# Optimization experiments

Hardware: AMD Instinct MI355X
Metric: run time of the kernel (lower is better)

The kernel has to match this reference:

```python
import jax, jax.numpy as jnp
import numpy as np

C = 128      # in_channels == global_graph_width
T = 1024     # time_step_len
B = 32       # batch (scenes)
N = B * T    # total nodes
E = 16 * N   # edges


def setup_inputs() -> dict:
    key = jax.random.key(0)
    ks = jax.random.split(key, 10)
    s = 1.0 / np.sqrt(C)
    return {
        "x": jax.random.normal(ks[0], (N, C), dtype=jnp.float32),
        "edge_index": jax.random.randint(ks[1], (2, E), 0, N, dtype=jnp.int64),
        "valid_lens": jax.random.randint(ks[2], (B,), 1, T, dtype=jnp.int64),
        "time_step_len": T,
        "Wq": jax.random.uniform(ks[3], (C, C), jnp.float32, -s, s),
        "bq": jax.random.uniform(ks[4], (C,), jnp.float32, -s, s),
        "Wk": jax.random.uniform(ks[5], (C, C), jnp.float32, -s, s),
        "bk": jax.random.uniform(ks[6], (C,), jnp.float32, -s, s),
        "Wv": jax.random.uniform(ks[7], (C, C), jnp.float32, -s, s),
        "bv": jax.random.uniform(ks[8], (C,), jnp.float32, -s, s),
    }


def reference(x, edge_index, valid_lens, time_step_len, Wq, bq, Wk, bk, Wv, bv):
    # GlobalGraph.forward in eval mode (no random training mask), 1 layer.
    n_nodes, c = x.shape
    xr = x.reshape(-1, time_step_len, c)                    # [B, T, C]
    q = xr @ Wq.T + bq                                      # [B, T, C]
    k = xr @ Wk.T + bk
    v = xr @ Wv.T + bv
    scores = jnp.einsum("btc,bsc->bts", q, k)               # [B, T, T]
    # masked_softmax: each row (b, t) keeps first valid_lens[b] cols, rest -1e6
    col = jnp.arange(time_step_len)                         # [T]
    mask = col[None, None, :] < valid_lens[:, None, None]   # [B, 1, T]
    scores = jnp.where(mask, scores, -1000000.0)
    attn = jax.nn.softmax(scores, axis=-1)                  # [B, T, T]
    out = jnp.einsum("bts,bsc->btc", attn, v).reshape(-1, c)  # [N, C]
    # MessagePassing propagate, aggr='add', flow source_to_target:
    # out_i = sum_{(j->i) in edges} out_j
    src, dst = edge_index[0], edge_index[1]
    return jax.ops.segment_sum(out[src], dst, num_segments=n_nodes)
```

## Files before the change

### kernel.cpp

```cpp
#include <hip/hip_runtime.h>
#include <hip/hip_bf16.h>
#include <stdint.h>

typedef __attribute__((ext_vector_type(8))) short short8;
typedef __attribute__((ext_vector_type(4))) float f32x4;

static constexpr int NN = 32768;
static constexpr int CC = 128;
static constexpr int TT = 1024;
static constexpr int BB = 32;
static constexpr int EE = 524288;
static constexpr int PAD = 96;
static constexpr int SCH = 512;

__device__ __forceinline__ unsigned short f2b(float f) {
    uint32_t u = __builtin_bit_cast(uint32_t, f);
    u = (u + 0x7fffu + ((u >> 16) & 1u)) >> 16;
    return (unsigned short)u;
}
__device__ __forceinline__ float b2f(unsigned short u) {
    uint32_t v = ((uint32_t)u) << 16;
    return __builtin_bit_cast(float, v);
}

__global__ __launch_bounds__(256) void k_cvtfill(
    const float* __restrict__ Wq, const float* __restrict__ Wk,
    const float* __restrict__ Wv, unsigned short* __restrict__ Wb,
    const int* __restrict__ ei, int* __restrict__ cnt, int* __restrict__ slot)
{
    if (blockIdx.x < 192) {
        int i = blockIdx.x * 256 + threadIdx.x;
        const float* w = (i < CC*CC) ? Wq : ((i < 2*CC*CC) ? Wk : Wv);
        Wb[i] = f2b(w[i & (CC*CC - 1)]);
    } else {
        int e = (blockIdx.x - 192) * 256 + threadIdx.x;
        int src = ei[e];
        int dst = ei[EE + e];
        int pos = atomicAdd(&cnt[dst], 1);
        if (pos < PAD) slot[(size_t)dst * PAD + pos] = src;
    }
}

static constexpr int QP = 132;

__global__ __launch_bounds__(256) void k_qkv(
    const float* __restrict__ x, const unsigned short* __restrict__ Wb,
    const float* __restrict__ bq, const float* __restrict__ bk, const float* __restrict__ bv,
    unsigned short* __restrict__ Qb, unsigned short* __restrict__ Kb,
    unsigned short* __restrict__ VB)
{
    __shared__ unsigned short qsm[4][16 * QP];
    int wv   = threadIdx.x >> 6;
    int wid  = (blockIdx.x << 2) + wv;
    int lane = threadIdx.x & 63;
    int l15  = lane & 15, quad = lane >> 4;
    int m0   = wid << 4;
    unsigned short* myT = qsm[wv];

    short8 a[4];
    const float* xrow = x + (size_t)(m0 + l15) * CC + quad * 8;
#pragma unroll
    for (int kk = 0; kk < 4; kk++) {
        float4 f0 = *(const float4*)(xrow + kk * 32);
        float4 f1 = *(const float4*)(xrow + kk * 32 + 4);
        short8 v;
        v[0] = (short)f2b(f0.x); v[1] = (short)f2b(f0.y);
        v[2] = (short)f2b(f0.z); v[3] = (short)f2b(f0.w);
        v[4] = (short)f2b(f1.x); v[5] = (short)f2b(f1.y);
        v[6] = (short)f2b(f1.z); v[7] = (short)f2b(f1.w);
        a[kk] = v;
    }

    for (int w2 = 0; w2 < 2; w2++) {
        const float* bias = w2 ? bk : bq;
        for (int nt = 0; nt < 8; nt++) {
            int n0 = nt << 4;
            const unsigned short* wbase = Wb + w2 * (CC*CC) + (size_t)(n0 + l15) * CC + quad * 8;
            f32x4 acc = {0.f, 0.f, 0.f, 0.f};
#pragma unroll
            for (int kk = 0; kk < 4; kk++) {
                short8 bfrag = *(const short8*)(wbase + kk * 32);
                acc = __builtin_amdgcn_mfma_f32_16x16x32_bf16(a[kk], bfrag, acc, 0, 0, 0);
            }
            float bval = bias[n0 + l15];
#pragma unroll
            for (int r = 0; r < 4; r++)
                myT[(quad * 4 + r) * QP + n0 + l15] = f2b(acc[r] + bval);
        }
        unsigned short* dstp = w2 ? Kb : Qb;
#pragma unroll
        for (int t = 0; t < 4; t++) {
            int g   = t * 64 + lane;
            int row = g >> 4;
            int gc  = (g & 15) * 8;
            short8 vv = *(const short8*)&myT[row * QP + gc];
            *(short8*)&dstp[(size_t)(m0 + row) * CC + gc] = vv;
        }
    }

    for (int nt = 0; nt < 8; nt++) {
        int n0 = nt << 4;
        const unsigned short* wbase = Wb + 2 * (CC*CC) + (size_t)(n0 + l15) * CC + quad * 8;
        f32x4 acc = {0.f, 0.f, 0.f, 0.f};
#pragma unroll
        for (int kk = 0; kk < 4; kk++) {
            short8 bfrag = *(const short8*)(wbase + kk * 32);
            acc = __builtin_amdgcn_mfma_f32_16x16x32_bf16(a[kk], bfrag, acc, 0, 0, 0);
        }
        float bval = bv[n0 + l15];
        int col = n0 + l15;
        ushort4 pk;
        pk.x = f2b(acc[0] + bval); pk.y = f2b(acc[1] + bval);
        pk.z = f2b(acc[2] + bval); pk.w = f2b(acc[3] + bval);
        int b_  = m0 >> 10;
        int sb  = (m0 & (TT - 1)) >> 5;
        int sin = (m0 & 31) + quad * 4;
        *(ushort4*)&VB[((size_t)(b_ * 32 + sb) * CC + col) * 32 + sin] = pk;
    }
}

static constexpr int PITCH = 40;

__global__ __launch_bounds__(512) void k_attn(
    const unsigned short* __restrict__ Qb, const unsigned short* __restrict__ Kb,
    const unsigned short* __restrict__ VB, const int* __restrict__ valid_lens,
    float* __restrict__ ao_a, float* __restrict__ ao_b,
    float* __restrict__ l0, float* __restrict__ l1,
    unsigned short* __restrict__ ao2)
{
    __shared__ unsigned short Ksm[2][512 * 8];
    __shared__ unsigned short Vsm[2][512 * 8];
    __shared__ unsigned short pl[8][16 * PITCH];

    int w    = threadIdx.x >> 6;
    int lane = threadIdx.x & 63;
    int l15  = lane & 15, quad = lane >> 4;
    int bid   = blockIdx.x;
    int qt8   = bid & 7;
    int chunk = (bid >> 3) & 1;
    int b     = bid >> 4;
    int m0    = b * TT + qt8 * 128 + w * 16;
    int L     = valid_lens[b];
    int sbeg  = chunk * SCH;
    if (sbeg >= L) return;
    int send  = min(L, sbeg + SCH);
    int nsteps = (send - sbeg + 31) >> 5;
    bool excl = (L <= SCH);

    int g    = (w << 6) | lane;
    int ksr  = g >> 4,  ksc = ((g & 15) - ksr) & 15;
    int vch  = g >> 2,  vsg = ((g & 3) - (vch >> 1)) & 3;

    const unsigned short* Kbase = Kb + (size_t)b * TT * CC;
    const unsigned short* Vbase = VB + (size_t)b * 32 * CC * 32;

#define STAGE(bufi, s0g)                                                              \
    do {                                                                              \
        int _s0 = (s0g);                                                              \
        __builtin_amdgcn_global_load_lds(                                             \
            (const __attribute__((address_space(1))) uint32_t*)(Kbase + (size_t)(_s0 + ksr) * CC + ksc * 8), \
            (__attribute__((address_space(3))) uint32_t*)&Ksm[bufi][(size_t)(w << 6) * 8], 16, 0, 0);        \
        const unsigned short* _vt = Vbase + (size_t)(_s0 >> 5) * CC * 32;             \
        __builtin_amdgcn_global_load_lds(                                             \
            (const __attribute__((address_space(1))) uint32_t*)(_vt + vch * 32 + vsg * 8),                   \
            (__attribute__((address_space(3))) uint32_t*)&Vsm[bufi][(size_t)(w << 6) * 8], 16, 0, 0);        \
    } while (0)

    short8 a[4];
    const unsigned short* qrow = Qb + (size_t)(m0 + l15) * CC + quad * 8;
#pragma unroll
    for (int kk = 0; kk < 4; kk++) a[kk] = *(const short8*)(qrow + kk * 32);

    f32x4 o[8];
#pragma unroll
    for (int ct = 0; ct < 8; ct++) o[ct] = (f32x4){0.f, 0.f, 0.f, 0.f};
    float l_[4] = {0.f, 0.f, 0.f, 0.f};

    unsigned short* myP = pl[w];

    STAGE(0, sbeg);
    for (int i = 0; i < nsteps; i++) {
        int s0 = sbeg + (i << 5);
        int bufi = i & 1;
        __syncthreads();
        if (i + 1 < nsteps) STAGE(1 - bufi, s0 + 32);

        const unsigned short* Kc = Ksm[bufi];
        const unsigned short* Vc = Vsm[bufi];

        f32x4 S0 = {0.f,0.f,0.f,0.f}, S1 = {0.f,0.f,0.f,0.f};
#pragma unroll
        for (int kk = 0; kk < 4; kk++) {
            int cidx = kk * 4 + quad;
            int sl0 = l15,      t0 = (cidx + sl0) & 15;
            int sl1 = 16 | l15, t1 = (cidx + sl1) & 15;
            short8 b0 = *(const short8*)&Kc[(size_t)(sl0 * 16 + t0) * 8];
            short8 b1 = *(const short8*)&Kc[(size_t)(sl1 * 16 + t1) * 8];
            S0 = __builtin_amdgcn_mfma_f32_16x16x32_bf16(a[kk], b0, S0, 0, 0, 0);
            S1 = __builtin_amdgcn_mfma_f32_16x16x32_bf16(a[kk], b1, S1, 0, 0, 0);
        }
        bool ok0 = (s0 + l15) < L;
        bool ok1 = (s0 + 16 + l15) < L;
        float p0[4], p1[4];
#pragma unroll
        for (int r = 0; r < 4; r++) {
            p0[r] = ok0 ? __expf(S0[r]) : 0.f;
            p1[r] = ok1 ? __expf(S1[r]) : 0.f;
            l_[r] += p0[r] + p1[r];
        }
#pragma unroll
        for (int r = 0; r < 4; r++) {
            int row = quad * 4 + r;
            myP[row * PITCH + l15]      = f2b(p0[r]);
            myP[row * PITCH + 16 + l15] = f2b(p1[r]);
        }
        short8 pf = *(const short8*)(myP + l15 * PITCH + quad * 8);
#pragma unroll
        for (int ct = 0; ct < 8; ct++) {
            int c  = (ct << 4) | l15;
            int sg = (quad + (c >> 1)) & 3;
            short8 vf = *(const short8*)&Vc[(size_t)(c * 4 + sg) * 8];
            o[ct] = __builtin_amdgcn_mfma_f32_16x16x32_bf16(pf, vf, o[ct], 0, 0, 0);
        }
    }

#pragma unroll
    for (int r = 0; r < 4; r++) {
#pragma unroll
        for (int off = 1; off < 16; off <<= 1) l_[r] += __shfl_xor(l_[r], off, 16);
    }

    if (excl) {
        float rl[4];
#pragma unroll
        for (int r = 0; r < 4; r++) rl[r] = 1.0f / l_[r];
#pragma unroll
        for (int ct = 0; ct < 8; ct++)
#pragma unroll
            for (int r = 0; r < 4; r++)
                ao2[(size_t)(m0 + quad * 4 + r) * CC + ct * 16 + l15] = f2b(o[ct][r] * rl[r]);
    } else {
        float* aoP = chunk ? ao_b : ao_a;
        float* lP  = chunk ? l1 : l0;
#pragma unroll
        for (int ct = 0; ct < 8; ct++)
#pragma unroll
            for (int r = 0; r < 4; r++)
                aoP[(size_t)(m0 + quad * 4 + r) * CC + ct * 16 + l15] = o[ct][r];
        if (l15 < 4) lP[m0 + quad * 4 + l15] = l_[l15];
    }
#undef STAGE
}

__global__ __launch_bounds__(256) void k_norm(
    const float* __restrict__ ao_a, const float* __restrict__ ao_b,
    const float* __restrict__ l0, const float* __restrict__ l1,
    const int* __restrict__ valid_lens, unsigned short* __restrict__ ao2)
{
    int i = blockIdx.x * 256 + threadIdx.x;
    int row = i >> 5;
    if (valid_lens[row >> 10] <= SCH) return;
    f32x4 va = ((const f32x4*)ao_a)[i];
    f32x4 vb = ((const f32x4*)ao_b)[i];
    float rl = 1.0f / (l0[row] + l1[row]);
    ushort4 u;
    u.x = f2b((va[0] + vb[0]) * rl); u.y = f2b((va[1] + vb[1]) * rl);
    u.z = f2b((va[2] + vb[2]) * rl); u.w = f2b((va[3] + vb[3]) * rl);
    ((ushort4*)ao2)[i] = u;
}

__global__ __launch_bounds__(256) void k_gather(
    const int* __restrict__ cnt, const int* __restrict__ slot,
    const unsigned short* __restrict__ ao2, float* __restrict__ out)
{
    int node = __builtin_amdgcn_readfirstlane(blockIdx.x * 4 + (threadIdx.x >> 6));
    int lane = threadIdx.x & 63;
    int g    = lane >> 4;
    int l15  = lane & 15;
    int deg  = min(cnt[node], PAD);
    const int* sl = slot + (size_t)node * PAD;
    const short8* base = (const short8*)ao2;

    float acc[8] = {0.f, 0.f, 0.f, 0.f, 0.f, 0.f, 0.f, 0.f};
    int full = deg >> 2;
    for (int t = 0; t < full; t++) {
        int src = sl[(t << 2) | g];
        short8 v = base[(size_t)src * 16 + l15];
#pragma unroll
        for (int c = 0; c < 8; c++) acc[c] += b2f((unsigned short)v[c]);
    }
    int rem = deg & 3;
    if (rem) {
        bool ok = g < rem;
        int idx = (full << 2) + (ok ? g : 0);
        int src = sl[idx];
        short8 v = base[(size_t)src * 16 + l15];
        if (ok) {
#pragma unroll
            for (int c = 0; c < 8; c++) acc[c] += b2f((unsigned short)v[c]);
        }
    }
#pragma unroll
    for (int c = 0; c < 8; c++) {
        acc[c] += __shfl_xor(acc[c], 16);
        acc[c] += __shfl_xor(acc[c], 32);
    }
    float* orow = out + (size_t)node * CC + l15 * 8;
    if (g == 0) {
        float4 lo; lo.x = acc[0]; lo.y = acc[1]; lo.z = acc[2]; lo.w = acc[3];
        *(float4*)orow = lo;
    } else if (g == 1) {
        float4 hi; hi.x = acc[4]; hi.y = acc[5]; hi.z = acc[6]; hi.w = acc[7];
        *(float4*)(orow + 4) = hi;
    }
}

extern "C" void kernel_launch(void* const* d_in, const int* in_sizes, int n_in,
                              void* d_out, int out_size, void* d_ws, size_t ws_size,
                              hipStream_t stream) {
    const float* x  = (const float*)d_in[0];
    const int*   ei = (const int*)d_in[1];
    const int*   vl = (const int*)d_in[2];
    const float* Wq = (const float*)d_in[4];
    const float* bq = (const float*)d_in[5];
    const float* Wk = (const float*)d_in[6];
    const float* bk = (const float*)d_in[7];
    const float* Wv = (const float*)d_in[8];
    const float* bv = (const float*)d_in[9];

    char* ws = (char*)d_ws;
    unsigned short* Wb   = (unsigned short*)(ws + 8388608);
    unsigned short* Qb   = (unsigned short*)(ws + 8486912);
    unsigned short* Kb   = (unsigned short*)(ws + 16875520);
    unsigned short* VB   = (unsigned short*)(ws + 25264128);
    float*          ao_a = (float*)(ws + 33652736);
    float*          ao_b = (float*)(ws + 50429952);
    float*          l0   = (float*)(ws + 67207168);
    float*          l1   = (float*)(ws + 67338240);
    unsigned short* ao2  = (unsigned short*)(ws + 67469312);
    int*            slot = (int*)(ws + 75857920);
    int*            cnt  = (int*)(ws + 88440832);
    float*          out  = (float*)d_out;

    hipMemsetAsync(cnt, 0, (size_t)NN * sizeof(int), stream);
    k_cvtfill<<<192 + EE/256, 256, 0, stream>>>(Wq, Wk, Wv, Wb, ei, cnt, slot);
    k_qkv    <<<NN/64,        256, 0, stream>>>(x, Wb, bq, bk, bv, Qb, Kb, VB);
    k_attn   <<<BB*8*2,       512, 0, stream>>>(Qb, Kb, VB, vl, ao_a, ao_b, l0, l1, ao2);
    k_norm   <<<NN*CC/4/256,  256, 0, stream>>>(ao_a, ao_b, l0, l1, vl, ao2);
    k_gather <<<NN/4,         256, 0, stream>>>(cnt, slot, ao2, out);
}
```

Before: 193.6 us.

## Give each attention wave two query tiles and halve block size

The attention kernel now runs 4 waves of 256 threads instead of 8, and each wave handles 32 query rows (two 16-row tiles). Each K and V fragment read from shared memory therefore feeds two MFMAs, halving LDS fragment reads per unit of work, and each thread issues two async staging loads. MFMA sections are wrapped in s_setprio to favour matrix issue. The cost is roughly double the accumulator registers per wave and fewer waves per block to hide latency.

```diff
diff --git a/kernel.cpp b/kernel.cpp
--- a/kernel.cpp
+++ b/kernel.cpp
@@ -121,7 +121,7 @@
 
 static constexpr int PITCH = 40;
 
-__global__ __launch_bounds__(512) void k_attn(
+__global__ __launch_bounds__(256, 2) void k_attn(
     const unsigned short* __restrict__ Qb, const unsigned short* __restrict__ Kb,
     const unsigned short* __restrict__ VB, const int* __restrict__ valid_lens,
     float* __restrict__ ao_a, float* __restrict__ ao_b,
@@ -130,7 +130,7 @@
 {
     __shared__ unsigned short Ksm[2][512 * 8];
     __shared__ unsigned short Vsm[2][512 * 8];
-    __shared__ unsigned short pl[8][16 * PITCH];
+    __shared__ unsigned short pl[4][2][16 * PITCH];
 
     int w    = threadIdx.x >> 6;
     int lane = threadIdx.x & 63;
@@ -139,7 +139,7 @@
     int qt8   = bid & 7;
     int chunk = (bid >> 3) & 1;
     int b     = bid >> 4;
-    int m0    = b * TT + qt8 * 128 + w * 16;
+    int m0    = b * TT + qt8 * 128 + w * 32;
     int L     = valid_lens[b];
     int sbeg  = chunk * SCH;
     if (sbeg >= L) return;
@@ -160,23 +160,39 @@
         __builtin_amdgcn_global_load_lds(                                             \
             (const __attribute__((address_space(1))) uint32_t*)(Kbase + (size_t)(_s0 + ksr) * CC + ksc * 8), \
             (__attribute__((address_space(3))) uint32_t*)&Ksm[bufi][(size_t)(w << 6) * 8], 16, 0, 0);        \
+        __builtin_amdgcn_global_load_lds(                                             \
+            (const __attribute__((address_space(1))) uint32_t*)(Kbase + (size_t)(_s0 + 16 + ksr) * CC + ksc * 8), \
+            (__attribute__((address_space(3))) uint32_t*)&Ksm[bufi][(size_t)((w << 6) + 256) * 8], 16, 0, 0);     \
         const unsigned short* _vt = Vbase + (size_t)(_s0 >> 5) * CC * 32;             \
         __builtin_amdgcn_global_load_lds(                                             \
             (const __attribute__((address_space(1))) uint32_t*)(_vt + vch * 32 + vsg * 8),                   \
             (__attribute__((address_space(3))) uint32_t*)&Vsm[bufi][(size_t)(w << 6) * 8], 16, 0, 0);        \
+        __builtin_amdgcn_global_load_lds(                                             \
+            (const __attribute__((address_space(1))) uint32_t*)(_vt + (vch + 64) * 32 + vsg * 8),            \
+            (__attribute__((address_space(3))) uint32_t*)&Vsm[bufi][(size_t)((w << 6) + 256) * 8], 16, 0, 0);     \
     } while (0)
 
-    short8 a[4];
-    const unsigned short* qrow = Qb + (size_t)(m0 + l15) * CC + quad * 8;
-#pragma unroll
-    for (int kk = 0; kk < 4; kk++) a[kk] = *(const short8*)(qrow + kk * 32);
-
-    f32x4 o[8];
-#pragma unroll
-    for (int ct = 0; ct < 8; ct++) o[ct] = (f32x4){0.f, 0.f, 0.f, 0.f};
-    float l_[4] = {0.f, 0.f, 0.f, 0.f};
-
-    unsigned short* myP = pl[w];
+    short8 a0[4], a1[4];
+    {
+        const unsigned short* qrow = Qb + (size_t)(m0 + l15) * CC + quad * 8;
+#pragma unroll
+        for (int kk = 0; kk < 4; kk++) a0[kk] = *(const short8*)(qrow + kk * 32);
+        qrow += 16 * CC;
+#pragma unroll
+        for (int kk = 0; kk < 4; kk++) a1[kk] = *(const short8*)(qrow + kk * 32);
+    }
+
+    f32x4 oa[8], ob[8];
+#pragma unroll
+    for (int ct = 0; ct < 8; ct++) {
+        oa[ct] = (f32x4){0.f, 0.f, 0.f, 0.f};
+        ob[ct] = (f32x4){0.f, 0.f, 0.f, 0.f};
+    }
+    float la[4] = {0.f, 0.f, 0.f, 0.f};
+    float lb[4] = {0.f, 0.f, 0.f, 0.f};
+
+    unsigned short* myPa = pl[w][0];
+    unsigned short* myPb = pl[w][1];
 
     STAGE(0, sbeg);
     for (int i = 0; i < nsteps; i++) {
@@ -188,66 +204,90 @@
         const unsigned short* Kc = Ksm[bufi];
         const unsigned short* Vc = Vsm[bufi];
 
-        f32x4 S0 = {0.f,0.f,0.f,0.f}, S1 = {0.f,0.f,0.f,0.f};
+        f32x4 S0a = {0.f,0.f,0.f,0.f}, S1a = {0.f,0.f,0.f,0.f};
+        f32x4 S0b = {0.f,0.f,0.f,0.f}, S1b = {0.f,0.f,0.f,0.f};
+        __builtin_amdgcn_s_setprio(1);
 #pragma unroll
         for (int kk = 0; kk < 4; kk++) {
             int cidx = kk * 4 + quad;
-            int sl0 = l15,      t0 = (cidx + sl0) & 15;
-            int sl1 = 16 | l15, t1 = (cidx + sl1) & 15;
-            short8 b0 = *(const short8*)&Kc[(size_t)(sl0 * 16 + t0) * 8];
-            short8 b1 = *(const short8*)&Kc[(size_t)(sl1 * 16 + t1) * 8];
-            S0 = __builtin_amdgcn_mfma_f32_16x16x32_bf16(a[kk], b0, S0, 0, 0, 0);
-            S1 = __builtin_amdgcn_mfma_f32_16x16x32_bf16(a[kk], b1, S1, 0, 0, 0);
-        }
+            int t0 = (cidx + l15) & 15;
+            short8 b0 = *(const short8*)&Kc[(size_t)(l15 * 16 + t0) * 8];
+            short8 b1 = *(const short8*)&Kc[(size_t)(((16 | l15) * 16) + t0) * 8];
+            S0a = __builtin_amdgcn_mfma_f32_16x16x32_bf16(a0[kk], b0, S0a, 0, 0, 0);
+            S1a = __builtin_amdgcn_mfma_f32_16x16x32_bf16(a0[kk], b1, S1a, 0, 0, 0);
+            S0b = __builtin_amdgcn_mfma_f32_16x16x32_bf16(a1[kk], b0, S0b, 0, 0, 0);
+            S1b = __builtin_amdgcn_mfma_f32_16x16x32_bf16(a1[kk], b1, S1b, 0, 0, 0);
+        }
+        __builtin_amdgcn_s_setprio(0);
+
         bool ok0 = (s0 + l15) < L;
         bool ok1 = (s0 + 16 + l15) < L;
-        float p0[4], p1[4];
+        float p0a[4], p1a[4], p0b[4], p1b[4];
 #pragma unroll
         for (int r = 0; r < 4; r++) {
-            p0[r] = ok0 ? __expf(S0[r]) : 0.f;
-            p1[r] = ok1 ? __expf(S1[r]) : 0.f;
-            l_[r] += p0[r] + p1[r];
+            p0a[r] = ok0 ? __expf(S0a[r]) : 0.f;
+            p1a[r] = ok1 ? __expf(S1a[r]) : 0.f;
+            p0b[r] = ok0 ? __expf(S0b[r]) : 0.f;
+            p1b[r] = ok1 ? __expf(S1b[r]) : 0.f;
+            la[r] += p0a[r] + p1a[r];
+            lb[r] += p0b[r] + p1b[r];
         }
 #pragma unroll
         for (int r = 0; r < 4; r++) {
             int row = quad * 4 + r;
-            myP[row * PITCH + l15]      = f2b(p0[r]);
-            myP[row * PITCH + 16 + l15] = f2b(p1[r]);
-        }
-        short8 pf = *(const short8*)(myP + l15 * PITCH + quad * 8);
+            myPa[row * PITCH + l15]      = f2b(p0a[r]);
+            myPa[row * PITCH + 16 + l15] = f2b(p1a[r]);
+            myPb[row * PITCH + l15]      = f2b(p0b[r]);
+            myPb[row * PITCH + 16 + l15] = f2b(p1b[r]);
+        }
+        short8 pfa = *(const short8*)(myPa + l15 * PITCH + quad * 8);
+        short8 pfb = *(const short8*)(myPb + l15 * PITCH + quad * 8);
+        __builtin_amdgcn_s_setprio(1);
 #pragma unroll
         for (int ct = 0; ct < 8; ct++) {
             int c  = (ct << 4) | l15;
             int sg = (quad + (c >> 1)) & 3;
             short8 vf = *(const short8*)&Vc[(size_t)(c * 4 + sg) * 8];
-            o[ct] = __builtin_amdgcn_mfma_f32_16x16x32_bf16(pf, vf, o[ct], 0, 0, 0);
-        }
+            oa[ct] = __builtin_amdgcn_mfma_f32_16x16x32_bf16(pfa, vf, oa[ct], 0, 0, 0);
+            ob[ct] = __builtin_amdgcn_mfma_f32_16x16x32_bf16(pfb, vf, ob[ct], 0, 0, 0);
+        }
+        __builtin_amdgcn_s_setprio(0);
     }
 
 #pragma unroll
     for (int r = 0; r < 4; r++) {
 #pragma unroll
-        for (int off = 1; off < 16; off <<= 1) l_[r] += __shfl_xor(l_[r], off, 16);
+        for (int off = 1; off < 16; off <<= 1) {
+            la[r] += __shfl_xor(la[r], off, 16);
+            lb[r] += __shfl_xor(lb[r], off, 16);
+        }
     }
 
     if (excl) {
-        float rl[4];
-#pragma unroll
-        for (int r = 0; r < 4; r++) rl[r] = 1.0f / l_[r];
+        float rla[4], rlb[4];
+#pragma unroll
+        for (int r = 0; r < 4; r++) { rla[r] = 1.0f / la[r]; rlb[r] = 1.0f / lb[r]; }
 #pragma unroll
         for (int ct = 0; ct < 8; ct++)
 #pragma unroll
-            for (int r = 0; r < 4; r++)
-                ao2[(size_t)(m0 + quad * 4 + r) * CC + ct * 16 + l15] = f2b(o[ct][r] * rl[r]);
+            for (int r = 0; r < 4; r++) {
+                ao2[(size_t)(m0 + quad * 4 + r) * CC + ct * 16 + l15]      = f2b(oa[ct][r] * rla[r]);
+                ao2[(size_t)(m0 + 16 + quad * 4 + r) * CC + ct * 16 + l15] = f2b(ob[ct][r] * rlb[r]);
+            }
     } else {
         float* aoP = chunk ? ao_b : ao_a;
         float* lP  = chunk ? l1 : l0;
 #pragma unroll
         for (int ct = 0; ct < 8; ct++)
 #pragma unroll
-            for (int r = 0; r < 4; r++)
-                aoP[(size_t)(m0 + quad * 4 + r) * CC + ct * 16 + l15] = o[ct][r];
-        if (l15 < 4) lP[m0 + quad * 4 + l15] = l_[l15];
+            for (int r = 0; r < 4; r++) {
+                aoP[(size_t)(m0 + quad * 4 + r) * CC + ct * 16 + l15]      = oa[ct][r];
+                aoP[(size_t)(m0 + 16 + quad * 4 + r) * CC + ct * 16 + l15] = ob[ct][r];
+            }
+        if (l15 < 4) {
+            lP[m0 + quad * 4 + l15]      = la[l15];
+            lP[m0 + 16 + quad * 4 + l15] = lb[l15];
+        }
     }
 #undef STAGE
 }
@@ -345,7 +385,7 @@
     hipMemsetAsync(cnt, 0, (size_t)NN * sizeof(int), stream);
     k_cvtfill<<<192 + EE/256, 256, 0, stream>>>(Wq, Wk, Wv, Wb, ei, cnt, slot);
     k_qkv    <<<NN/64,        256, 0, stream>>>(x, Wb, bq, bk, bv, Qb, Kb, VB);
-    k_attn   <<<BB*8*2,       512, 0, stream>>>(Qb, Kb, VB, vl, ao_a, ao_b, l0, l1, ao2);
+    k_attn   <<<BB*8*2,       256, 0, stream>>>(Qb, Kb, VB, vl, ao_a, ao_b, l0, l1, ao2);
     k_norm   <<<NN*CC/4/256,  256, 0, stream>>>(ao_a, ao_b, l0, l1, vl, ao2);
     k_gather <<<NN/4,         256, 0, stream>>>(cnt, slot, ao2, out);
 }
```

New measurement: 193.5 us. Within noise of the previous version (-0.0%).
